# Performance work log

Measured on AMD Instinct MI355X. Metric: run time of the kernel, lower is better.

## Reference

```python
import jax, jax.numpy as jnp
import numpy as np

NUM_ATOMS = 65536
NUM_BONDS = 131072          # directed bonds; row NUM_BONDS is the zero sentinel h(-1)
MAX_NBR = 4
ATOM_FDIM = 133
CONCAT_FDIM = 147           # atom_fdim + bond_fdim
D_HIDDEN = 300
DEPTH = 3
GF_DIM = 2048
N_MOLS = 4096               # uniform molecules: 16 atoms each


def setup_inputs() -> dict:
    key = jax.random.key(0)
    ks = jax.random.split(key, 9)
    atom_features = jax.random.normal(ks[0], (NUM_ATOMS, ATOM_FDIM), dtype=jnp.float32)
    f_ini_atoms_bonds = jax.random.normal(ks[1], (NUM_BONDS + 1, CONCAT_FDIM), dtype=jnp.float32)
    f_ini_atoms_bonds = f_ini_atoms_bonds.at[-1].set(0.0)  # h(-1) sentinel row
    # indices in [-1, NUM_BONDS-1]; -1 means 'no incoming bond' -> sentinel
    mapping = jax.random.randint(ks[2], (NUM_BONDS + 1, MAX_NBR), -1, NUM_BONDS)
    mapping = mapping.at[-1].set(-1)
    atom_to_incoming_bonds = jax.random.randint(ks[3], (NUM_ATOMS, MAX_NBR), -1, NUM_BONDS)
    global_features = jax.random.normal(ks[4], (N_MOLS, GF_DIM), dtype=jnp.float32)
    W_i = jax.random.normal(ks[5], (D_HIDDEN, CONCAT_FDIM), dtype=jnp.float32) / np.sqrt(CONCAT_FDIM)
    W_h = jax.random.normal(ks[6], (D_HIDDEN, D_HIDDEN), dtype=jnp.float32) / np.sqrt(D_HIDDEN)
    W_o = jax.random.normal(ks[7], (D_HIDDEN, ATOM_FDIM + D_HIDDEN), dtype=jnp.float32) / np.sqrt(ATOM_FDIM + D_HIDDEN)
    b_o = jax.random.normal(ks[8], (D_HIDDEN,), dtype=jnp.float32) * 0.01
    return {
        'atom_features': atom_features,
        'f_ini_atoms_bonds': f_ini_atoms_bonds,
        'atom_to_incoming_bonds': atom_to_incoming_bonds,
        'mapping': mapping,
        'global_features': global_features,
        'W_i': W_i, 'W_h': W_h, 'W_o': W_o, 'b_o': b_o,
    }


def reference(atom_features, f_ini_atoms_bonds, atom_to_incoming_bonds, mapping,
              global_features, W_i, W_h, W_o, b_o):
    nb1 = f_ini_atoms_bonds.shape[0]          # num_bonds + 1 (last row = zero sentinel)
    sentinel = nb1 - 1
    # -1 padding indexes the zero sentinel row (torch negative-index trick)
    map_idx = jnp.where(mapping < 0, sentinel, mapping)
    a2b_idx = jnp.where(atom_to_incoming_bonds < 0, sentinel, atom_to_incoming_bonds)

    inp = f_ini_atoms_bonds @ W_i.T           # [nb1, d_hidden]
    h_message = jax.nn.relu(inp)
    for _ in range(1, DEPTH):                 # depth-1 message passing steps
        message = h_message[map_idx].sum(axis=1)          # gather-sum over incoming bonds
        h_message = jax.nn.relu(inp + message @ W_h.T)    # (dropout p=0 omitted)

    # atom readout: sum incoming bond hidden states per atom
    messages = h_message[a2b_idx].sum(axis=1)             # [num_atoms, d_hidden]
    atoms_hidden = jax.nn.relu(
        jnp.concatenate([atom_features, messages], axis=1) @ W_o.T + b_o)

    # mean readout per molecule (uniform molecule size)
    n_mols = global_features.shape[0]
    d = atoms_hidden.shape[-1]
    mol_vecs = atoms_hidden.reshape(n_mols, -1, d).mean(axis=1)
    return jnp.concatenate([mol_vecs, global_features], axis=1)
```

## Files before the change

kernel.cpp:

```cpp
#include <hip/hip_runtime.h>

typedef short bf16x8 __attribute__((ext_vector_type(8)));
typedef float f32x4 __attribute__((ext_vector_type(4)));

constexpr int NB1    = 131073;
constexpr int SENT   = 131072;
constexpr int NATOMS = 65536;
constexpr int AFD    = 133;
constexpr int CFD    = 147;
constexpr int DH     = 300;
constexpr int GFD    = 2048;
constexpr int NMOLS  = 4096;
constexpr int OUTD   = DH + GFD;
constexpr int HS     = 320;
constexpr int KP1    = 160;
constexpr int KP2    = 320;
constexpr int KPC    = 480;

__device__ __forceinline__ unsigned short f2b(float f) {
    unsigned u = __float_as_uint(f);
    u += 0x7fffu + ((u >> 16) & 1u);
    return (unsigned short)(u >> 16);
}
__device__ __forceinline__ float blo(unsigned x) { return __uint_as_float(x << 16); }
__device__ __forceinline__ float bhi(unsigned x) { return __uint_as_float(x & 0xffff0000u); }
__device__ __forceinline__ unsigned pk2(float hi, float lo) {
    return ((unsigned)f2b(hi) << 16) | (unsigned)f2b(lo);
}
__device__ __forceinline__ unsigned pairsum4(unsigned a, unsigned b, unsigned c, unsigned d) {
    float lo = blo(a) + blo(b) + blo(c) + blo(d);
    float hi = bhi(a) + bhi(b) + bhi(c) + bhi(d);
    return pk2(hi, lo);
}
__device__ __forceinline__ unsigned relu_pk(unsigned u) {
    unsigned lo = (u & 0x8000u) ? 0u : (u & 0xFFFFu);
    unsigned hi = (u & 0x80000000u) ? 0u : (u & 0xFFFF0000u);
    return lo | hi;
}
__device__ __forceinline__ uint4 relu4(uint4 v) {
    v.x = relu_pk(v.x); v.y = relu_pk(v.y); v.z = relu_pk(v.z); v.w = relu_pk(v.w);
    return v;
}
__device__ __forceinline__ bf16x8 asbf(uint4 u) {
    union { uint4 u; bf16x8 b; } c; c.u = u; return c.b;
}

__device__ __forceinline__ void mfma_step(const short* __restrict__ A, const uint4 (&B)[5],
                                          int ml, int kl, f32x4 (&acc)[4][5]) {
    bf16x8 af[4];
#pragma unroll
    for (int mt = 0; mt < 4; ++mt)
        af[mt] = *(const bf16x8*)&A[(kl * 64 + mt * 16 + ml) * 8];
#pragma unroll
    for (int mt = 0; mt < 4; ++mt)
#pragma unroll
        for (int nt = 0; nt < 5; ++nt)
            acc[mt][nt] = __builtin_amdgcn_mfma_f32_16x16x32_bf16(af[mt], asbf(B[nt]), acc[mt][nt], 0, 0, 0);
}


__global__ __launch_bounds__(256, 3) void gemm1(
    const float* __restrict__ fini,
    const unsigned short* __restrict__ WiP,
    unsigned short* __restrict__ inp)
{
    __shared__ __align__(16) short As[2][4 * 64 * 8];
    const int tid = threadIdx.x, w = tid >> 6, lane = tid & 63;
    const int ml = lane & 15, kl = lane >> 4;
    const int sr = tid & 63, seg = tid >> 6;
    const int m0 = blockIdx.x * 64;
    const bool mok = (m0 + sr) < NB1;
    const float* fp = fini + (size_t)(mok ? m0 + sr : SENT) * CFD;
    const unsigned short* bp = WiP + (size_t)(w * 80 + ml) * KP1 + kl * 8;

    f32x4 acc[4][5];
#pragma unroll
    for (int mt = 0; mt < 4; ++mt)
#pragma unroll
        for (int nt = 0; nt < 5; ++nt) acc[mt][nt] = (f32x4){0.f, 0.f, 0.f, 0.f};

    {
        union { short s[8]; uint4 u; } st;
#pragma unroll
        for (int j = 0; j < 8; ++j) {
            int k = seg * 8 + j;
            st.s[j] = (short)f2b((mok && k < CFD) ? fp[k] : 0.f);
        }
        *(uint4*)&As[0][(seg * 64 + sr) * 8] = st.u;
    }
    uint4 Bcur[5];
#pragma unroll
    for (int nt = 0; nt < 5; ++nt) Bcur[nt] = *(const uint4*)(bp + nt * 16 * KP1);
    __syncthreads();

    for (int c = 0; c < 5; ++c) {
        const int cn = c + 1;
        float vn[8]; uint4 Bn[5];
        if (cn < 5) {
#pragma unroll
            for (int j = 0; j < 8; ++j) {
                int k = cn * 32 + seg * 8 + j;
                vn[j] = (mok && k < CFD) ? fp[k] : 0.f;
            }
#pragma unroll
            for (int nt = 0; nt < 5; ++nt) Bn[nt] = *(const uint4*)(bp + cn * 32 + nt * 16 * KP1);
        }
        mfma_step(As[c & 1], Bcur, ml, kl, acc);
        if (cn < 5) {
            union { short s[8]; uint4 u; } st;
#pragma unroll
            for (int j = 0; j < 8; ++j) st.s[j] = (short)f2b(vn[j]);
            *(uint4*)&As[cn & 1][(seg * 64 + sr) * 8] = st.u;
#pragma unroll
            for (int nt = 0; nt < 5; ++nt) Bcur[nt] = Bn[nt];
        }
        __syncthreads();
    }
#pragma unroll
    for (int mt = 0; mt < 4; ++mt)
#pragma unroll
        for (int reg = 0; reg < 4; ++reg) {
            int m = m0 + mt * 16 + kl * 4 + reg;
            if (m < NB1) {
#pragma unroll
                for (int nt = 0; nt < 5; ++nt)
                    inp[(size_t)m * HS + w * 80 + nt * 16 + ml] = f2b(acc[mt][nt][reg]);
            }
        }
}

__global__ __launch_bounds__(256, 3) void ygemm(
    const unsigned short* __restrict__ src,
    const unsigned short* __restrict__ Wh,
    unsigned short* __restrict__ y,
    int relu_stage)
{
    __shared__ __align__(16) short As[2][4 * 64 * 8];
    const int tid = threadIdx.x, w = tid >> 6, lane = tid & 63;
    const int ml = lane & 15, kl = lane >> 4;
    const int sr = tid & 63, seg = tid >> 6;
    const int m0 = blockIdx.x * 64;
    const int srow = (m0 + sr) < NB1 ? (m0 + sr) : SENT;
    const unsigned short* ap = src + (size_t)srow * HS + seg * 8;
    const unsigned short* bp = Wh + (size_t)(w * 80 + ml) * KP2 + kl * 8;

    f32x4 acc[4][5];
#pragma unroll
    for (int mt = 0; mt < 4; ++mt)
#pragma unroll
        for (int nt = 0; nt < 5; ++nt) acc[mt][nt] = (f32x4){0.f, 0.f, 0.f, 0.f};

    {
        uint4 av = *(const uint4*)ap;
        if (relu_stage) av = relu4(av);
        *(uint4*)&As[0][(seg * 64 + sr) * 8] = av;
    }
    uint4 Bcur[5];
#pragma unroll
    for (int nt = 0; nt < 5; ++nt) Bcur[nt] = *(const uint4*)(bp + nt * 16 * KP2);
    __syncthreads();

    for (int c = 0; c < 10; ++c) {
        uint4 an; uint4 Bn[5];
        if (c < 9) {
            an = *(const uint4*)(ap + (c + 1) * 32);
#pragma unroll
            for (int nt = 0; nt < 5; ++nt)
                Bn[nt] = *(const uint4*)(bp + (c + 1) * 32 + nt * 16 * KP2);
        }
        mfma_step(As[c & 1], Bcur, ml, kl, acc);
        if (c < 9) {
            if (relu_stage) an = relu4(an);
            *(uint4*)&As[(c + 1) & 1][(seg * 64 + sr) * 8] = an;
#pragma unroll
            for (int nt = 0; nt < 5; ++nt) Bcur[nt] = Bn[nt];
        }
        __syncthreads();
    }
#pragma unroll
    for (int mt = 0; mt < 4; ++mt)
#pragma unroll
        for (int reg = 0; reg < 4; ++reg) {
            int m = m0 + mt * 16 + kl * 4 + reg;
            if (m < NB1) {
#pragma unroll
                for (int nt = 0; nt < 5; ++nt)
                    y[(size_t)m * HS + w * 80 + nt * 16 + ml] = f2b(acc[mt][nt][reg]);
            }
        }
}

__global__ __launch_bounds__(256) void gather_bond(
    const unsigned short* __restrict__ y, const unsigned short* __restrict__ inp,
    const int* __restrict__ mapping, unsigned short* __restrict__ hout)
{
    int t = blockIdx.x * 256 + threadIdx.x;
    int row = t >> 3, g = t & 7;
    if (row >= NB1) return;
    int4 mp = *(const int4*)(mapping + (size_t)row * 4);
    const unsigned short* r0 = y + (size_t)(mp.x < 0 ? SENT : mp.x) * HS;
    const unsigned short* r1 = y + (size_t)(mp.y < 0 ? SENT : mp.y) * HS;
    const unsigned short* r2 = y + (size_t)(mp.z < 0 ? SENT : mp.z) * HS;
    const unsigned short* r3 = y + (size_t)(mp.w < 0 ? SENT : mp.w) * HS;
    const unsigned short* ip = inp + (size_t)row * HS;
    unsigned short* op = hout + (size_t)row * HS;
#pragma unroll
    for (int s = 0; s < 5; ++s) {
        int off = (g + s * 8) * 8;
        uint4 a = *(const uint4*)(r0 + off);
        uint4 b = *(const uint4*)(r1 + off);
        uint4 c = *(const uint4*)(r2 + off);
        uint4 d = *(const uint4*)(r3 + off);
        uint4 e = *(const uint4*)(ip + off);
        uint4 o;
        {
            float lo, hi;
            lo = blo(a.x)+blo(b.x)+blo(c.x)+blo(d.x)+blo(e.x); hi = bhi(a.x)+bhi(b.x)+bhi(c.x)+bhi(d.x)+bhi(e.x);
            o.x = pk2(hi > 0.f ? hi : 0.f, lo > 0.f ? lo : 0.f);
            lo = blo(a.y)+blo(b.y)+blo(c.y)+blo(d.y)+blo(e.y); hi = bhi(a.y)+bhi(b.y)+bhi(c.y)+bhi(d.y)+bhi(e.y);
            o.y = pk2(hi > 0.f ? hi : 0.f, lo > 0.f ? lo : 0.f);
            lo = blo(a.z)+blo(b.z)+blo(c.z)+blo(d.z)+blo(e.z); hi = bhi(a.z)+bhi(b.z)+bhi(c.z)+bhi(d.z)+bhi(e.z);
            o.z = pk2(hi > 0.f ? hi : 0.f, lo > 0.f ? lo : 0.f);
            lo = blo(a.w)+blo(b.w)+blo(c.w)+blo(d.w)+blo(e.w); hi = bhi(a.w)+bhi(b.w)+bhi(c.w)+bhi(d.w)+bhi(e.w);
            o.w = pk2(hi > 0.f ? hi : 0.f, lo > 0.f ? lo : 0.f);
        }
        *(uint4*)(op + off) = o;
    }
}

__global__ __launch_bounds__(256) void gather_atom(
    const unsigned short* __restrict__ h, const int* __restrict__ a2b,
    unsigned short* __restrict__ msg)
{
    int t = blockIdx.x * 256 + threadIdx.x;
    int row = t >> 3, g = t & 7;
    int4 mp = *(const int4*)(a2b + (size_t)row * 4);
    const unsigned short* r0 = h + (size_t)(mp.x < 0 ? SENT : mp.x) * HS;
    const unsigned short* r1 = h + (size_t)(mp.y < 0 ? SENT : mp.y) * HS;
    const unsigned short* r2 = h + (size_t)(mp.z < 0 ? SENT : mp.z) * HS;
    const unsigned short* r3 = h + (size_t)(mp.w < 0 ? SENT : mp.w) * HS;
    unsigned short* op = msg + (size_t)row * HS;
#pragma unroll
    for (int s = 0; s < 5; ++s) {
        int off = (g + s * 8) * 8;
        uint4 a = *(const uint4*)(r0 + off);
        uint4 b = *(const uint4*)(r1 + off);
        uint4 c = *(const uint4*)(r2 + off);
        uint4 d = *(const uint4*)(r3 + off);
        uint4 o;
        o.x = pairsum4(a.x, b.x, c.x, d.x);
        o.y = pairsum4(a.y, b.y, c.y, d.y);
        o.z = pairsum4(a.z, b.z, c.z, d.z);
        o.w = pairsum4(a.w, b.w, c.w, d.w);
        *(uint4*)(op + off) = o;
    }
}

__global__ __launch_bounds__(256, 3) void atom_gemm(
    const float* __restrict__ atomf,
    const unsigned short* __restrict__ msg,
    const unsigned short* __restrict__ WoC,
    const float* __restrict__ bo,
    float* __restrict__ out)
{
    __shared__ __align__(16) short As[2][4 * 64 * 8];
    const int tid = threadIdx.x, w = tid >> 6, lane = tid & 63;
    const int ml = lane & 15, kl = lane >> 4;
    const int sr = tid & 63, seg = tid >> 6;
    const int m0 = blockIdx.x * 64;
    const float* fp = atomf + (size_t)(m0 + sr) * AFD;
    const unsigned short* mp = msg + (size_t)(m0 + sr) * HS + seg * 8;
    const unsigned short* bp = WoC + (size_t)(w * 80 + ml) * KPC + kl * 8;

    f32x4 acc[4][5];
#pragma unroll
    for (int mt = 0; mt < 4; ++mt)
#pragma unroll
        for (int nt = 0; nt < 5; ++nt) acc[mt][nt] = (f32x4){0.f, 0.f, 0.f, 0.f};

    {
        union { short s[8]; uint4 u; } st;
#pragma unroll
        for (int j = 0; j < 8; ++j) {
            int k = seg * 8 + j;
            st.s[j] = (short)f2b(k < AFD ? fp[k] : 0.f);
        }
        *(uint4*)&As[0][(seg * 64 + sr) * 8] = st.u;
    }
    uint4 Bcur[5];
#pragma unroll
    for (int nt = 0; nt < 5; ++nt) Bcur[nt] = *(const uint4*)(bp + nt * 16 * KPC);
    __syncthreads();

    for (int c = 0; c < 15; ++c) {
        const int cn = c + 1;
        float vn[8]; uint4 an; uint4 Bn[5];
        if (cn < 15) {
            if (cn < 5) {
#pragma unroll
                for (int j = 0; j < 8; ++j) {
                    int k = cn * 32 + seg * 8 + j;
                    vn[j] = (k < AFD) ? fp[k] : 0.f;
                }
            } else {
                an = *(const uint4*)(mp + (cn - 5) * 32);
            }
#pragma unroll
            for (int nt = 0; nt < 5; ++nt) Bn[nt] = *(const uint4*)(bp + cn * 32 + nt * 16 * KPC);
        }
        mfma_step(As[c & 1], Bcur, ml, kl, acc);
        if (cn < 15) {
            if (cn < 5) {
                union { short s[8]; uint4 u; } st;
#pragma unroll
                for (int j = 0; j < 8; ++j) st.s[j] = (short)f2b(vn[j]);
                *(uint4*)&As[cn & 1][(seg * 64 + sr) * 8] = st.u;
            } else {
                *(uint4*)&As[cn & 1][(seg * 64 + sr) * 8] = an;
            }
#pragma unroll
            for (int nt = 0; nt < 5; ++nt) Bcur[nt] = Bn[nt];
        }
        __syncthreads();
    }

#pragma unroll
    for (int mt = 0; mt < 4; ++mt) {
        int mol = blockIdx.x * 4 + mt;
#pragma unroll
        for (int nt = 0; nt < 5; ++nt) {
            int n = w * 80 + nt * 16 + ml;
            float bias = (n < DH) ? bo[n] : 0.f;
            float s = 0.f;
#pragma unroll
            for (int reg = 0; reg < 4; ++reg) {
                float v = acc[mt][nt][reg] + bias;
                s += (v > 0.f ? v : 0.f);
            }
            s += __shfl_down(s, 32, 64);
            s += __shfl_down(s, 16, 64);
            if (kl == 0 && n < DH) out[(size_t)mol * OUTD + n] = s * (1.f / 16.f);
        }
    }
}


__global__ __launch_bounds__(256, 3) void bond_gemm_fb(
    const float* __restrict__ fini, const unsigned short* __restrict__ finiB,
    const unsigned short* __restrict__ hsrc, const int* __restrict__ mapping,
    const unsigned short* __restrict__ WiP, const unsigned short* __restrict__ WhP,
    unsigned short* __restrict__ hdst, int do_msg, int useB)
{
    const int tid = threadIdx.x, wv = tid >> 6, lane = tid & 63;
    const int ml = lane & 15, kh = lane >> 4;
    const int m0 = blockIdx.x * 64 + wv * 16;
    const int mrow = m0 + ml;
    const int mrowc = mrow < NB1 ? mrow : SENT;

    f32x4 acc[20];
#pragma unroll
    for (int nt = 0; nt < 20; ++nt) acc[nt] = (f32x4){0.f, 0.f, 0.f, 0.f};

    if (useB) {
        const unsigned short* fb = finiB + (size_t)mrowc * KP1 + kh * 8;
#pragma unroll
        for (int c = 0; c < 5; ++c) {
            bf16x8 af = *(const bf16x8*)(fb + c * 32);
            const unsigned short* bp = WiP + ml * KP1 + c * 32 + kh * 8;
#pragma unroll
            for (int nt = 0; nt < 20; ++nt)
                acc[nt] = __builtin_amdgcn_mfma_f32_16x16x32_bf16(af, *(const bf16x8*)(bp + nt * 16 * KP1), acc[nt], 0, 0, 0);
        }
    } else {
        const float* fp = fini + (size_t)mrowc * CFD;
#pragma unroll
        for (int c = 0; c < 5; ++c) {
            union { short s[8]; bf16x8 x; } u;
#pragma unroll
            for (int j = 0; j < 8; ++j) {
                int k = c * 32 + kh * 8 + j;
                u.s[j] = (short)f2b(k < CFD ? fp[k] : 0.f);
            }
            const unsigned short* bp = WiP + ml * KP1 + c * 32 + kh * 8;
#pragma unroll
            for (int nt = 0; nt < 20; ++nt)
                acc[nt] = __builtin_amdgcn_mfma_f32_16x16x32_bf16(u.x, *(const bf16x8*)(bp + nt * 16 * KP1), acc[nt], 0, 0, 0);
        }
    }
    if (do_msg) {
        int4 mp = *(const int4*)(mapping + (size_t)mrowc * 4);
        const unsigned short* g0 = hsrc + (size_t)(mp.x < 0 ? SENT : mp.x) * HS + kh * 8;
        const unsigned short* g1 = hsrc + (size_t)(mp.y < 0 ? SENT : mp.y) * HS + kh * 8;
        const unsigned short* g2 = hsrc + (size_t)(mp.z < 0 ? SENT : mp.z) * HS + kh * 8;
        const unsigned short* g3 = hsrc + (size_t)(mp.w < 0 ? SENT : mp.w) * HS + kh * 8;
#pragma unroll
        for (int c = 0; c < 10; ++c) {
            uint4 a = *(const uint4*)(g0 + c * 32);
            uint4 b = *(const uint4*)(g1 + c * 32);
            uint4 cc = *(const uint4*)(g2 + c * 32);
            uint4 d = *(const uint4*)(g3 + c * 32);
            uint4 o;
            o.x = pairsum4(a.x, b.x, cc.x, d.x);
            o.y = pairsum4(a.y, b.y, cc.y, d.y);
            o.z = pairsum4(a.z, b.z, cc.z, d.z);
            o.w = pairsum4(a.w, b.w, cc.w, d.w);
            const unsigned short* bp = WhP + ml * KP2 + c * 32 + kh * 8;
#pragma unroll
            for (int nt = 0; nt < 20; ++nt)
                acc[nt] = __builtin_amdgcn_mfma_f32_16x16x32_bf16(asbf(o), *(const bf16x8*)(bp + nt * 16 * KP2), acc[nt], 0, 0, 0);
        }
    }
#pragma unroll
    for (int nt = 0; nt < 20; ++nt) {
        int n = nt * 16 + ml;
#pragma unroll
        for (int reg = 0; reg < 4; ++reg) {
            int m = m0 + kh * 4 + reg;
            if (m < NB1) {
                float v = acc[nt][reg];
                hdst[(size_t)m * HS + n] = f2b(v > 0.f ? v : 0.f);
            }
        }
    }
}

__global__ __launch_bounds__(256, 3) void atom_gemm_fb(
    const float* __restrict__ atomf, const unsigned short* __restrict__ hsrc,
    const int* __restrict__ a2b, const unsigned short* __restrict__ WoA,
    const unsigned short* __restrict__ WoB, const float* __restrict__ bo,
    float* __restrict__ out)
{
    const int tid = threadIdx.x, wv = tid >> 6, lane = tid & 63;
    const int ml = lane & 15, kh = lane >> 4;
    const int m0 = blockIdx.x * 64 + wv * 16;
    const int arow = m0 + ml;

    f32x4 acc[20];
#pragma unroll
    for (int nt = 0; nt < 20; ++nt) acc[nt] = (f32x4){0.f, 0.f, 0.f, 0.f};
    {
        const float* fp = atomf + (size_t)arow * AFD;
#pragma unroll
        for (int c = 0; c < 5; ++c) {
            union { short s[8]; bf16x8 x; } u;
#pragma unroll
            for (int j = 0; j < 8; ++j) {
                int k = c * 32 + kh * 8 + j;
                u.s[j] = (short)f2b(k < AFD ? fp[k] : 0.f);
            }
            const unsigned short* bp = WoA + ml * KP1 + c * 32 + kh * 8;
#pragma unroll
            for (int nt = 0; nt < 20; ++nt)
                acc[nt] = __builtin_amdgcn_mfma_f32_16x16x32_bf16(u.x, *(const bf16x8*)(bp + nt * 16 * KP1), acc[nt], 0, 0, 0);
        }
    }
    {
        int4 mp = *(const int4*)(a2b + (size_t)arow * 4);
        const unsigned short* g0 = hsrc + (size_t)(mp.x < 0 ? SENT : mp.x) * HS + kh * 8;
        const unsigned short* g1 = hsrc + (size_t)(mp.y < 0 ? SENT : mp.y) * HS + kh * 8;
        const unsigned short* g2 = hsrc + (size_t)(mp.z < 0 ? SENT : mp.z) * HS + kh * 8;
        const unsigned short* g3 = hsrc + (size_t)(mp.w < 0 ? SENT : mp.w) * HS + kh * 8;
#pragma unroll
        for (int c = 0; c < 10; ++c) {
            uint4 a = *(const uint4*)(g0 + c * 32);
            uint4 b = *(const uint4*)(g1 + c * 32);
            uint4 cc = *(const uint4*)(g2 + c * 32);
            uint4 d = *(const uint4*)(g3 + c * 32);
            uint4 o;
            o.x = pairsum4(a.x, b.x, cc.x, d.x);
            o.y = pairsum4(a.y, b.y, cc.y, d.y);
            o.z = pairsum4(a.z, b.z, cc.z, d.z);
            o.w = pairsum4(a.w, b.w, cc.w, d.w);
            const unsigned short* bp = WoB + ml * KP2 + c * 32 + kh * 8;
#pragma unroll
            for (int nt = 0; nt < 20; ++nt)
                acc[nt] = __builtin_amdgcn_mfma_f32_16x16x32_bf16(asbf(o), *(const bf16x8*)(bp + nt * 16 * KP2), acc[nt], 0, 0, 0);
        }
    }
    const int mol = blockIdx.x * 4 + wv;
#pragma unroll
    for (int nt = 0; nt < 20; ++nt) {
        int n = nt * 16 + ml;
        float bias = (n < DH) ? bo[n] : 0.f;
        float s = 0.f;
#pragma unroll
        for (int reg = 0; reg < 4; ++reg) {
            float v = acc[nt][reg] + bias;
            s += (v > 0.f ? v : 0.f);
        }
        s += __shfl_down(s, 32, 64);
        s += __shfl_down(s, 16, 64);
        if (kh == 0 && n < DH) out[(size_t)mol * OUTD + n] = s * (1.f / 16.f);
    }
}

__global__ void prep_fini(const float* __restrict__ fini, unsigned short* __restrict__ finiB) {
    int t = blockIdx.x * blockDim.x + threadIdx.x;
    if (t >= NB1 * 20) return;
    int row = t / 20, g = t % 20;
    const float* src = fini + (size_t)row * CFD;
    union { unsigned short s[8]; uint4 u; } o;
#pragma unroll
    for (int j = 0; j < 8; ++j) {
        int k = g * 8 + j;
        o.s[j] = (k < CFD) ? f2b(src[k]) : (unsigned short)0;
    }
    *(uint4*)(finiB + (size_t)row * KP1 + g * 8) = o.u;
}


__global__ void prep_w(const float* __restrict__ Wi, const float* __restrict__ Wh,
                       const float* __restrict__ Wo, unsigned short* __restrict__ wb, int mode) {
    int t = blockIdx.x * blockDim.x + threadIdx.x;
    if (t >= 307200) return;
    float v = 0.f;
    if (t < 51200) {
        int n = t / 160, k = t % 160;
        if (n < DH && k < CFD) v = Wi[n * CFD + k];
    } else if (t < 153600) {
        int q = t - 51200; int n = q / 320, k = q % 320;
        if (n < DH && k < DH) v = Wh[n * DH + k];
    } else if (mode) {
        int q = t - 153600; int n = q / 480, k = q % 480;
        if (n < DH) {
            if (k < AFD) v = Wo[n * 433 + k];
            else if (k >= 160 && k < 460) v = Wo[n * 433 + AFD + (k - 160)];
        }
    } else if (t < 204800) {
        int q = t - 153600; int n = q / 160, k = q % 160;
        if (n < DH && k < AFD) v = Wo[n * 433 + k];
    } else {
        int q = t - 204800; int n = q / 320, k = q % 320;
        if (n < DH && k < DH) v = Wo[n * 433 + AFD + k];
    }
    wb[t] = f2b(v);
}

__global__ void copy_gf(const float4* __restrict__ gf, float* __restrict__ out) {
    int t = blockIdx.x * blockDim.x + threadIdx.x;
    if (t >= NMOLS * (GFD / 4)) return;
    int mol = t >> 9;
    int g4 = t & 511;
    float4 v = gf[t];
    *(float4*)(out + (size_t)mol * OUTD + DH + g4 * 4) = v;
}

extern "C" void kernel_launch(void* const* d_in, const int* in_sizes, int n_in,
                              void* d_out, int out_size, void* d_ws, size_t ws_size,
                              hipStream_t stream) {
    const float* atomf   = (const float*)d_in[0];
    const float* fini    = (const float*)d_in[1];
    const int*   a2b     = (const int*)d_in[2];
    const int*   mapping = (const int*)d_in[3];
    const float* gf      = (const float*)d_in[4];
    const float* W_i     = (const float*)d_in[5];
    const float* W_h     = (const float*)d_in[6];
    const float* W_o     = (const float*)d_in[7];
    const float* b_o     = (const float*)d_in[8];
    float* out = (float*)d_out;

    char* ws = (char*)d_ws;
    size_t SA = (((size_t)NB1 * HS * 2) + 255) & ~(size_t)255;
    size_t SW = 307200 * 2;
    dim3 blk(256);

    if (ws_size >= 3 * SA + SW) {
        unsigned short* inp  = (unsigned short*)ws;
        unsigned short* bufA = (unsigned short*)(ws + SA);
        unsigned short* bufB = (unsigned short*)(ws + 2 * SA);
        unsigned short* wb   = (unsigned short*)(ws + 3 * SA);
        unsigned short* WiP = wb;
        unsigned short* WhP = wb + 51200;
        unsigned short* WoC = wb + 153600;
        unsigned short* msg = inp;

        prep_w<<<1200, blk, 0, stream>>>(W_i, W_h, W_o, wb, 1);
        gemm1<<<2049, blk, 0, stream>>>(fini, WiP, inp);
        ygemm<<<2049, blk, 0, stream>>>(inp, WhP, bufB, 1);
        gather_bond<<<4097, blk, 0, stream>>>(bufB, inp, mapping, bufA);
        ygemm<<<2049, blk, 0, stream>>>(bufA, WhP, bufB, 0);
        gather_bond<<<4097, blk, 0, stream>>>(bufB, inp, mapping, bufA);
        gather_atom<<<2048, blk, 0, stream>>>(bufA, a2b, msg);
        atom_gemm<<<1024, blk, 0, stream>>>(atomf, msg, WoC, b_o, out);
    } else {
        size_t SF = (size_t)NB1 * KP1 * 2;
        unsigned short* h_a = (unsigned short*)ws;
        unsigned short* h_b = (unsigned short*)(ws + SA);
        unsigned short* wb  = (unsigned short*)(ws + 2 * SA);
        unsigned short* finiB = (unsigned short*)(ws + 2 * SA + SW);
        unsigned short* WiP = wb;
        unsigned short* WhP = wb + 51200;
        unsigned short* WoA = wb + 153600;
        unsigned short* WoB = wb + 204800;
        int useB = (ws_size >= 2 * SA + SW + SF) ? 1 : 0;

        prep_w<<<1200, blk, 0, stream>>>(W_i, W_h, W_o, wb, 0);
        if (useB) prep_fini<<<(NB1 * 20 + 255) / 256, blk, 0, stream>>>(fini, finiB);
        bond_gemm_fb<<<2049, blk, 0, stream>>>(fini, finiB, h_a, mapping, WiP, WhP, h_a, 0, useB);
        bond_gemm_fb<<<2049, blk, 0, stream>>>(fini, finiB, h_a, mapping, WiP, WhP, h_b, 1, useB);
        bond_gemm_fb<<<2049, blk, 0, stream>>>(fini, finiB, h_b, mapping, WiP, WhP, h_a, 1, useB);
        atom_gemm_fb<<<1024, blk, 0, stream>>>(atomf, h_a, a2b, WoA, WoB, b_o, out);
    }
    copy_gf<<<NMOLS * (GFD / 4) / 256, blk, 0, stream>>>((const float4*)gf, out);
}
```

Baseline: 612.5 us.

## Fuse gathers and GEMMs into stage kernels with full-K shared-memory tiles

Merges the input projection with the first W_h GEMM, the first bond gather with the second W_h GEMM, and the atom gather with the output GEMM. Each fused kernel stages a full-K tile (padded stride) in LDS so intermediate message buffers no longer round-trip through global memory. This cuts the launch count and global traffic for two intermediate tensors. In exchange the larger LDS footprint lowers occupancy to 2 blocks per CU and drops the double-buffered prefetch. The fallback path also loses its bf16 pre-converted fini option.

```diff
diff --git a/kernel.cpp b/kernel.cpp
--- a/kernel.cpp
+++ b/kernel.cpp
@@ -16,6 +16,8 @@
 constexpr int KP1    = 160;
 constexpr int KP2    = 320;
 constexpr int KPC    = 480;
+constexpr int LSTR   = 328;
+constexpr int LSTRC  = 488;
 
 __device__ __forceinline__ unsigned short f2b(float f) {
     unsigned u = __float_as_uint(f);
@@ -32,46 +34,22 @@
     float hi = bhi(a) + bhi(b) + bhi(c) + bhi(d);
     return pk2(hi, lo);
 }
-__device__ __forceinline__ unsigned relu_pk(unsigned u) {
-    unsigned lo = (u & 0x8000u) ? 0u : (u & 0xFFFFu);
-    unsigned hi = (u & 0x80000000u) ? 0u : (u & 0xFFFF0000u);
-    return lo | hi;
-}
-__device__ __forceinline__ uint4 relu4(uint4 v) {
-    v.x = relu_pk(v.x); v.y = relu_pk(v.y); v.z = relu_pk(v.z); v.w = relu_pk(v.w);
-    return v;
-}
 __device__ __forceinline__ bf16x8 asbf(uint4 u) {
     union { uint4 u; bf16x8 b; } c; c.u = u; return c.b;
 }
 
-__device__ __forceinline__ void mfma_step(const short* __restrict__ A, const uint4 (&B)[5],
-                                          int ml, int kl, f32x4 (&acc)[4][5]) {
-    bf16x8 af[4];
-#pragma unroll
-    for (int mt = 0; mt < 4; ++mt)
-        af[mt] = *(const bf16x8*)&A[(kl * 64 + mt * 16 + ml) * 8];
-#pragma unroll
-    for (int mt = 0; mt < 4; ++mt)
-#pragma unroll
-        for (int nt = 0; nt < 5; ++nt)
-            acc[mt][nt] = __builtin_amdgcn_mfma_f32_16x16x32_bf16(af[mt], asbf(B[nt]), acc[mt][nt], 0, 0, 0);
-}
-
-
-__global__ __launch_bounds__(256, 3) void gemm1(
+
+__global__ __launch_bounds__(256, 2) void fused_in(
     const float* __restrict__ fini,
     const unsigned short* __restrict__ WiP,
-    unsigned short* __restrict__ inp)
+    const unsigned short* __restrict__ WhP,
+    unsigned short* __restrict__ inp,
+    unsigned short* __restrict__ y1)
 {
-    __shared__ __align__(16) short As[2][4 * 64 * 8];
+    __shared__ __align__(16) short As[64 * LSTR];
     const int tid = threadIdx.x, w = tid >> 6, lane = tid & 63;
     const int ml = lane & 15, kl = lane >> 4;
-    const int sr = tid & 63, seg = tid >> 6;
     const int m0 = blockIdx.x * 64;
-    const bool mok = (m0 + sr) < NB1;
-    const float* fp = fini + (size_t)(mok ? m0 + sr : SENT) * CFD;
-    const unsigned short* bp = WiP + (size_t)(w * 80 + ml) * KP1 + kl * 8;
 
     f32x4 acc[4][5];
 #pragma unroll
@@ -79,42 +57,76 @@
 #pragma unroll
         for (int nt = 0; nt < 5; ++nt) acc[mt][nt] = (f32x4){0.f, 0.f, 0.f, 0.f};
 
-    {
-        union { short s[8]; uint4 u; } st;
-#pragma unroll
-        for (int j = 0; j < 8; ++j) {
-            int k = seg * 8 + j;
-            st.s[j] = (short)f2b((mok && k < CFD) ? fp[k] : 0.f);
-        }
-        *(uint4*)&As[0][(seg * 64 + sr) * 8] = st.u;
-    }
-    uint4 Bcur[5];
-#pragma unroll
-    for (int nt = 0; nt < 5; ++nt) Bcur[nt] = *(const uint4*)(bp + nt * 16 * KP1);
+    const float* fr[4];
+#pragma unroll
+    for (int mt = 0; mt < 4; ++mt) {
+        int r = m0 + mt * 16 + ml;
+        fr[mt] = fini + (size_t)(r < NB1 ? r : SENT) * CFD + kl * 8;
+    }
+    const unsigned short* bpi = WiP + (size_t)(w * 80 + ml) * KP1 + kl * 8;
+#pragma unroll
+    for (int c = 0; c < 5; ++c) {
+        uint4 B[5];
+#pragma unroll
+        for (int nt = 0; nt < 5; ++nt) B[nt] = *(const uint4*)(bpi + c * 32 + nt * 16 * KP1);
+        bf16x8 af[4];
+#pragma unroll
+        for (int mt = 0; mt < 4; ++mt) {
+            union { short s[8]; bf16x8 x; } u;
+            if (c < 4) {
+#pragma unroll
+                for (int j = 0; j < 8; ++j) u.s[j] = (short)f2b(fr[mt][c * 32 + j]);
+            } else {
+#pragma unroll
+                for (int j = 0; j < 8; ++j) {
+                    int k = 128 + kl * 8 + j;
+                    u.s[j] = (short)f2b(k < CFD ? fr[mt][c * 32 + j] : 0.f);
+                }
+            }
+            af[mt] = u.x;
+        }
+#pragma unroll
+        for (int mt = 0; mt < 4; ++mt)
+#pragma unroll
+            for (int nt = 0; nt < 5; ++nt)
+                acc[mt][nt] = __builtin_amdgcn_mfma_f32_16x16x32_bf16(af[mt], asbf(B[nt]), acc[mt][nt], 0, 0, 0);
+    }
+
+#pragma unroll
+    for (int mt = 0; mt < 4; ++mt)
+#pragma unroll
+        for (int reg = 0; reg < 4; ++reg) {
+            int lr = mt * 16 + kl * 4 + reg;
+            int m = m0 + lr;
+#pragma unroll
+            for (int nt = 0; nt < 5; ++nt) {
+                int col = w * 80 + nt * 16 + ml;
+                float v = acc[mt][nt][reg];
+                if (m < NB1) inp[(size_t)m * HS + col] = f2b(v);
+                As[lr * LSTR + col] = (short)f2b(v > 0.f ? v : 0.f);
+            }
+        }
     __syncthreads();
 
-    for (int c = 0; c < 5; ++c) {
-        const int cn = c + 1;
-        float vn[8]; uint4 Bn[5];
-        if (cn < 5) {
-#pragma unroll
-            for (int j = 0; j < 8; ++j) {
-                int k = cn * 32 + seg * 8 + j;
-                vn[j] = (mok && k < CFD) ? fp[k] : 0.f;
-            }
-#pragma unroll
-            for (int nt = 0; nt < 5; ++nt) Bn[nt] = *(const uint4*)(bp + cn * 32 + nt * 16 * KP1);
-        }
-        mfma_step(As[c & 1], Bcur, ml, kl, acc);
-        if (cn < 5) {
-            union { short s[8]; uint4 u; } st;
-#pragma unroll
-            for (int j = 0; j < 8; ++j) st.s[j] = (short)f2b(vn[j]);
-            *(uint4*)&As[cn & 1][(seg * 64 + sr) * 8] = st.u;
-#pragma unroll
-            for (int nt = 0; nt < 5; ++nt) Bcur[nt] = Bn[nt];
-        }
-        __syncthreads();
+#pragma unroll
+    for (int mt = 0; mt < 4; ++mt)
+#pragma unroll
+        for (int nt = 0; nt < 5; ++nt) acc[mt][nt] = (f32x4){0.f, 0.f, 0.f, 0.f};
+    const unsigned short* bph = WhP + (size_t)(w * 80 + ml) * KP2 + kl * 8;
+#pragma unroll
+    for (int c = 0; c < 10; ++c) {
+        uint4 B[5];
+#pragma unroll
+        for (int nt = 0; nt < 5; ++nt) B[nt] = *(const uint4*)(bph + c * 32 + nt * 16 * KP2);
+        bf16x8 af[4];
+#pragma unroll
+        for (int mt = 0; mt < 4; ++mt)
+            af[mt] = *(const bf16x8*)&As[(mt * 16 + ml) * LSTR + c * 32 + kl * 8];
+#pragma unroll
+        for (int mt = 0; mt < 4; ++mt)
+#pragma unroll
+            for (int nt = 0; nt < 5; ++nt)
+                acc[mt][nt] = __builtin_amdgcn_mfma_f32_16x16x32_bf16(af[mt], asbf(B[nt]), acc[mt][nt], 0, 0, 0);
     }
 #pragma unroll
     for (int mt = 0; mt < 4; ++mt)
@@ -124,58 +136,76 @@
             if (m < NB1) {
 #pragma unroll
                 for (int nt = 0; nt < 5; ++nt)
-                    inp[(size_t)m * HS + w * 80 + nt * 16 + ml] = f2b(acc[mt][nt][reg]);
-            }
-        }
-}
-
-__global__ __launch_bounds__(256, 3) void ygemm(
-    const unsigned short* __restrict__ src,
-    const unsigned short* __restrict__ Wh,
-    unsigned short* __restrict__ y,
-    int relu_stage)
+                    y1[(size_t)m * HS + w * 80 + nt * 16 + ml] = f2b(acc[mt][nt][reg]);
+            }
+        }
+}
+
+__global__ __launch_bounds__(256, 2) void fused_mid(
+    const unsigned short* __restrict__ ysrc,
+    const unsigned short* __restrict__ inp,
+    const int* __restrict__ mapping,
+    const unsigned short* __restrict__ WhP,
+    unsigned short* __restrict__ ydst)
 {
-    __shared__ __align__(16) short As[2][4 * 64 * 8];
+    __shared__ __align__(16) short As[64 * LSTR];
     const int tid = threadIdx.x, w = tid >> 6, lane = tid & 63;
     const int ml = lane & 15, kl = lane >> 4;
-    const int sr = tid & 63, seg = tid >> 6;
     const int m0 = blockIdx.x * 64;
-    const int srow = (m0 + sr) < NB1 ? (m0 + sr) : SENT;
-    const unsigned short* ap = src + (size_t)srow * HS + seg * 8;
-    const unsigned short* bp = Wh + (size_t)(w * 80 + ml) * KP2 + kl * 8;
+
+    {
+        const int sr = tid & 63, sg = tid >> 6;
+        int srow = m0 + sr;
+        int crow = srow < NB1 ? srow : SENT;
+        int4 mp = *(const int4*)(mapping + (size_t)crow * 4);
+        const unsigned short* r0 = ysrc + (size_t)(mp.x < 0 ? SENT : mp.x) * HS;
+        const unsigned short* r1 = ysrc + (size_t)(mp.y < 0 ? SENT : mp.y) * HS;
+        const unsigned short* r2 = ysrc + (size_t)(mp.z < 0 ? SENT : mp.z) * HS;
+        const unsigned short* r3 = ysrc + (size_t)(mp.w < 0 ? SENT : mp.w) * HS;
+        const unsigned short* ip = inp + (size_t)crow * HS;
+#pragma unroll
+        for (int s = 0; s < 10; ++s) {
+            int off = (s * 4 + sg) * 8;
+            uint4 a = *(const uint4*)(r0 + off);
+            uint4 b = *(const uint4*)(r1 + off);
+            uint4 c = *(const uint4*)(r2 + off);
+            uint4 d = *(const uint4*)(r3 + off);
+            uint4 e = *(const uint4*)(ip + off);
+            uint4 o;
+            float lo, hi;
+            lo = blo(a.x)+blo(b.x)+blo(c.x)+blo(d.x)+blo(e.x); hi = bhi(a.x)+bhi(b.x)+bhi(c.x)+bhi(d.x)+bhi(e.x);
+            o.x = pk2(hi > 0.f ? hi : 0.f, lo > 0.f ? lo : 0.f);
+            lo = blo(a.y)+blo(b.y)+blo(c.y)+blo(d.y)+blo(e.y); hi = bhi(a.y)+bhi(b.y)+bhi(c.y)+bhi(d.y)+bhi(e.y);
+            o.y = pk2(hi > 0.f ? hi : 0.f, lo > 0.f ? lo : 0.f);
+            lo = blo(a.z)+blo(b.z)+blo(c.z)+blo(d.z)+blo(e.z); hi = bhi(a.z)+bhi(b.z)+bhi(c.z)+bhi(d.z)+bhi(e.z);
+            o.z = pk2(hi > 0.f ? hi : 0.f, lo > 0.f ? lo : 0.f);
+            lo = blo(a.w)+blo(b.w)+blo(c.w)+blo(d.w)+blo(e.w); hi = bhi(a.w)+bhi(b.w)+bhi(c.w)+bhi(d.w)+bhi(e.w);
+            o.w = pk2(hi > 0.f ? hi : 0.f, lo > 0.f ? lo : 0.f);
+            *(uint4*)&As[sr * LSTR + off] = o;
+        }
+    }
+    __syncthreads();
 
     f32x4 acc[4][5];
 #pragma unroll
     for (int mt = 0; mt < 4; ++mt)
 #pragma unroll
         for (int nt = 0; nt < 5; ++nt) acc[mt][nt] = (f32x4){0.f, 0.f, 0.f, 0.f};
-
-    {
-        uint4 av = *(const uint4*)ap;
-        if (relu_stage) av = relu4(av);
-        *(uint4*)&As[0][(seg * 64 + sr) * 8] = av;
-    }
-    uint4 Bcur[5];
-#pragma unroll
-    for (int nt = 0; nt < 5; ++nt) Bcur[nt] = *(const uint4*)(bp + nt * 16 * KP2);
-    __syncthreads();
-
+    const unsigned short* bph = WhP + (size_t)(w * 80 + ml) * KP2 + kl * 8;
+#pragma unroll
     for (int c = 0; c < 10; ++c) {
-        uint4 an; uint4 Bn[5];
-        if (c < 9) {
-            an = *(const uint4*)(ap + (c + 1) * 32);
+        uint4 B[5];
+#pragma unroll
+        for (int nt = 0; nt < 5; ++nt) B[nt] = *(const uint4*)(bph + c * 32 + nt * 16 * KP2);
+        bf16x8 af[4];
+#pragma unroll
+        for (int mt = 0; mt < 4; ++mt)
+            af[mt] = *(const bf16x8*)&As[(mt * 16 + ml) * LSTR + c * 32 + kl * 8];
+#pragma unroll
+        for (int mt = 0; mt < 4; ++mt)
 #pragma unroll
             for (int nt = 0; nt < 5; ++nt)
-                Bn[nt] = *(const uint4*)(bp + (c + 1) * 32 + nt * 16 * KP2);
-        }
-        mfma_step(As[c & 1], Bcur, ml, kl, acc);
-        if (c < 9) {
-            if (relu_stage) an = relu4(an);
-            *(uint4*)&As[(c + 1) & 1][(seg * 64 + sr) * 8] = an;
-#pragma unroll
-            for (int nt = 0; nt < 5; ++nt) Bcur[nt] = Bn[nt];
-        }
-        __syncthreads();
+                acc[mt][nt] = __builtin_amdgcn_mfma_f32_16x16x32_bf16(af[mt], asbf(B[nt]), acc[mt][nt], 0, 0, 0);
     }
 #pragma unroll
     for (int mt = 0; mt < 4; ++mt)
@@ -185,7 +215,7 @@
             if (m < NB1) {
 #pragma unroll
                 for (int nt = 0; nt < 5; ++nt)
-                    y[(size_t)m * HS + w * 80 + nt * 16 + ml] = f2b(acc[mt][nt][reg]);
+                    ydst[(size_t)m * HS + w * 80 + nt * 16 + ml] = f2b(acc[mt][nt][reg]);
             }
         }
 }
@@ -213,115 +243,89 @@
         uint4 d = *(const uint4*)(r3 + off);
         uint4 e = *(const uint4*)(ip + off);
         uint4 o;
-        {
-            float lo, hi;
-            lo = blo(a.x)+blo(b.x)+blo(c.x)+blo(d.x)+blo(e.x); hi = bhi(a.x)+bhi(b.x)+bhi(c.x)+bhi(d.x)+bhi(e.x);
-            o.x = pk2(hi > 0.f ? hi : 0.f, lo > 0.f ? lo : 0.f);
-            lo = blo(a.y)+blo(b.y)+blo(c.y)+blo(d.y)+blo(e.y); hi = bhi(a.y)+bhi(b.y)+bhi(c.y)+bhi(d.y)+bhi(e.y);
-            o.y = pk2(hi > 0.f ? hi : 0.f, lo > 0.f ? lo : 0.f);
-            lo = blo(a.z)+blo(b.z)+blo(c.z)+blo(d.z)+blo(e.z); hi = bhi(a.z)+bhi(b.z)+bhi(c.z)+bhi(d.z)+bhi(e.z);
-            o.z = pk2(hi > 0.f ? hi : 0.f, lo > 0.f ? lo : 0.f);
-            lo = blo(a.w)+blo(b.w)+blo(c.w)+blo(d.w)+blo(e.w); hi = bhi(a.w)+bhi(b.w)+bhi(c.w)+bhi(d.w)+bhi(e.w);
-            o.w = pk2(hi > 0.f ? hi : 0.f, lo > 0.f ? lo : 0.f);
-        }
+        float lo, hi;
+        lo = blo(a.x)+blo(b.x)+blo(c.x)+blo(d.x)+blo(e.x); hi = bhi(a.x)+bhi(b.x)+bhi(c.x)+bhi(d.x)+bhi(e.x);
+        o.x = pk2(hi > 0.f ? hi : 0.f, lo > 0.f ? lo : 0.f);
+        lo = blo(a.y)+blo(b.y)+blo(c.y)+blo(d.y)+blo(e.y); hi = bhi(a.y)+bhi(b.y)+bhi(c.y)+bhi(d.y)+bhi(e.y);
+        o.y = pk2(hi > 0.f ? hi : 0.f, lo > 0.f ? lo : 0.f);
+        lo = blo(a.z)+blo(b.z)+blo(c.z)+blo(d.z)+blo(e.z); hi = bhi(a.z)+bhi(b.z)+bhi(c.z)+bhi(d.z)+bhi(e.z);
+        o.z = pk2(hi > 0.f ? hi : 0.f, lo > 0.f ? lo : 0.f);
+        lo = blo(a.w)+blo(b.w)+blo(c.w)+blo(d.w)+blo(e.w); hi = bhi(a.w)+bhi(b.w)+bhi(c.w)+bhi(d.w)+bhi(e.w);
+        o.w = pk2(hi > 0.f ? hi : 0.f, lo > 0.f ? lo : 0.f);
         *(uint4*)(op + off) = o;
     }
 }
 
-__global__ __launch_bounds__(256) void gather_atom(
-    const unsigned short* __restrict__ h, const int* __restrict__ a2b,
-    unsigned short* __restrict__ msg)
-{
-    int t = blockIdx.x * 256 + threadIdx.x;
-    int row = t >> 3, g = t & 7;
-    int4 mp = *(const int4*)(a2b + (size_t)row * 4);
-    const unsigned short* r0 = h + (size_t)(mp.x < 0 ? SENT : mp.x) * HS;
-    const unsigned short* r1 = h + (size_t)(mp.y < 0 ? SENT : mp.y) * HS;
-    const unsigned short* r2 = h + (size_t)(mp.z < 0 ? SENT : mp.z) * HS;
-    const unsigned short* r3 = h + (size_t)(mp.w < 0 ? SENT : mp.w) * HS;
-    unsigned short* op = msg + (size_t)row * HS;
-#pragma unroll
-    for (int s = 0; s < 5; ++s) {
-        int off = (g + s * 8) * 8;
-        uint4 a = *(const uint4*)(r0 + off);
-        uint4 b = *(const uint4*)(r1 + off);
-        uint4 c = *(const uint4*)(r2 + off);
-        uint4 d = *(const uint4*)(r3 + off);
-        uint4 o;
-        o.x = pairsum4(a.x, b.x, c.x, d.x);
-        o.y = pairsum4(a.y, b.y, c.y, d.y);
-        o.z = pairsum4(a.z, b.z, c.z, d.z);
-        o.w = pairsum4(a.w, b.w, c.w, d.w);
-        *(uint4*)(op + off) = o;
-    }
-}
-
-__global__ __launch_bounds__(256, 3) void atom_gemm(
+__global__ __launch_bounds__(256, 2) void fused_atom(
     const float* __restrict__ atomf,
-    const unsigned short* __restrict__ msg,
+    const unsigned short* __restrict__ h,
+    const int* __restrict__ a2b,
     const unsigned short* __restrict__ WoC,
     const float* __restrict__ bo,
     float* __restrict__ out)
 {
-    __shared__ __align__(16) short As[2][4 * 64 * 8];
+    __shared__ __align__(16) short As[64 * LSTRC];
     const int tid = threadIdx.x, w = tid >> 6, lane = tid & 63;
     const int ml = lane & 15, kl = lane >> 4;
-    const int sr = tid & 63, seg = tid >> 6;
     const int m0 = blockIdx.x * 64;
-    const float* fp = atomf + (size_t)(m0 + sr) * AFD;
-    const unsigned short* mp = msg + (size_t)(m0 + sr) * HS + seg * 8;
+
+    {
+        const int sr = tid & 63, sg = tid >> 6;
+        int row = m0 + sr;
+        int4 mp = *(const int4*)(a2b + (size_t)row * 4);
+        const unsigned short* r0 = h + (size_t)(mp.x < 0 ? SENT : mp.x) * HS;
+        const unsigned short* r1 = h + (size_t)(mp.y < 0 ? SENT : mp.y) * HS;
+        const unsigned short* r2 = h + (size_t)(mp.z < 0 ? SENT : mp.z) * HS;
+        const unsigned short* r3 = h + (size_t)(mp.w < 0 ? SENT : mp.w) * HS;
+        const float* fp = atomf + (size_t)row * AFD;
+#pragma unroll
+        for (int s = 0; s < 15; ++s) {
+            int k0 = (s * 4 + sg) * 8;
+            if (k0 < KP1) {
+                union { short s8[8]; uint4 u; } u;
+#pragma unroll
+                for (int j = 0; j < 8; ++j) {
+                    int k = k0 + j;
+                    u.s8[j] = (short)f2b(k < AFD ? fp[k] : 0.f);
+                }
+                *(uint4*)&As[sr * LSTRC + k0] = u.u;
+            } else {
+                int off = k0 - KP1;
+                uint4 a = *(const uint4*)(r0 + off);
+                uint4 b = *(const uint4*)(r1 + off);
+                uint4 c = *(const uint4*)(r2 + off);
+                uint4 d = *(const uint4*)(r3 + off);
+                uint4 o;
+                o.x = pairsum4(a.x, b.x, c.x, d.x);
+                o.y = pairsum4(a.y, b.y, c.y, d.y);
+                o.z = pairsum4(a.z, b.z, c.z, d.z);
+                o.w = pairsum4(a.w, b.w, c.w, d.w);
+                *(uint4*)&As[sr * LSTRC + k0] = o;
+            }
+        }
+    }
+    __syncthreads();
+
+    f32x4 acc[4][5];
+#pragma unroll
+    for (int mt = 0; mt < 4; ++mt)
+#pragma unroll
+        for (int nt = 0; nt < 5; ++nt) acc[mt][nt] = (f32x4){0.f, 0.f, 0.f, 0.f};
     const unsigned short* bp = WoC + (size_t)(w * 80 + ml) * KPC + kl * 8;
-
-    f32x4 acc[4][5];
-#pragma unroll
-    for (int mt = 0; mt < 4; ++mt)
-#pragma unroll
-        for (int nt = 0; nt < 5; ++nt) acc[mt][nt] = (f32x4){0.f, 0.f, 0.f, 0.f};
-
-    {
-        union { short s[8]; uint4 u; } st;
-#pragma unroll
-        for (int j = 0; j < 8; ++j) {
-            int k = seg * 8 + j;
-            st.s[j] = (short)f2b(k < AFD ? fp[k] : 0.f);
-        }
-        *(uint4*)&As[0][(seg * 64 + sr) * 8] = st.u;
-    }
-    uint4 Bcur[5];
-#pragma unroll
-    for (int nt = 0; nt < 5; ++nt) Bcur[nt] = *(const uint4*)(bp + nt * 16 * KPC);
-    __syncthreads();
-
+#pragma unroll
     for (int c = 0; c < 15; ++c) {
-        const int cn = c + 1;
-        float vn[8]; uint4 an; uint4 Bn[5];
-        if (cn < 15) {
-            if (cn < 5) {
-#pragma unroll
-                for (int j = 0; j < 8; ++j) {
-                    int k = cn * 32 + seg * 8 + j;
-                    vn[j] = (k < AFD) ? fp[k] : 0.f;
-                }
-            } else {
-                an = *(const uint4*)(mp + (cn - 5) * 32);
-            }
-#pragma unroll
-            for (int nt = 0; nt < 5; ++nt) Bn[nt] = *(const uint4*)(bp + cn * 32 + nt * 16 * KPC);
-        }
-        mfma_step(As[c & 1], Bcur, ml, kl, acc);
-        if (cn < 15) {
-            if (cn < 5) {
-                union { short s[8]; uint4 u; } st;
-#pragma unroll
-                for (int j = 0; j < 8; ++j) st.s[j] = (short)f2b(vn[j]);
-                *(uint4*)&As[cn & 1][(seg * 64 + sr) * 8] = st.u;
-            } else {
-                *(uint4*)&As[cn & 1][(seg * 64 + sr) * 8] = an;
-            }
-#pragma unroll
-            for (int nt = 0; nt < 5; ++nt) Bcur[nt] = Bn[nt];
-        }
-        __syncthreads();
+        uint4 B[5];
+#pragma unroll
+        for (int nt = 0; nt < 5; ++nt) B[nt] = *(const uint4*)(bp + c * 32 + nt * 16 * KPC);
+        bf16x8 af[4];
+#pragma unroll
+        for (int mt = 0; mt < 4; ++mt)
+            af[mt] = *(const bf16x8*)&As[(mt * 16 + ml) * LSTRC + c * 32 + kl * 8];
+#pragma unroll
+        for (int mt = 0; mt < 4; ++mt)
+#pragma unroll
+            for (int nt = 0; nt < 5; ++nt)
+                acc[mt][nt] = __builtin_amdgcn_mfma_f32_16x16x32_bf16(af[mt], asbf(B[nt]), acc[mt][nt], 0, 0, 0);
     }
 
 #pragma unroll
@@ -346,10 +350,10 @@
 
 
 __global__ __launch_bounds__(256, 3) void bond_gemm_fb(
-    const float* __restrict__ fini, const unsigned short* __restrict__ finiB,
-    const unsigned short* __restrict__ hsrc, const int* __restrict__ mapping,
-    const unsigned short* __restrict__ WiP, const unsigned short* __restrict__ WhP,
-    unsigned short* __restrict__ hdst, int do_msg, int useB)
+    const float* __restrict__ fini, const unsigned short* __restrict__ hsrc,
+    const int* __restrict__ mapping, const unsigned short* __restrict__ WiP,
+    const unsigned short* __restrict__ WhP, unsigned short* __restrict__ hdst,
+    int do_msg)
 {
     const int tid = threadIdx.x, wv = tid >> 6, lane = tid & 63;
     const int ml = lane & 15, kh = lane >> 4;
@@ -360,18 +364,7 @@
     f32x4 acc[20];
 #pragma unroll
     for (int nt = 0; nt < 20; ++nt) acc[nt] = (f32x4){0.f, 0.f, 0.f, 0.f};
-
-    if (useB) {
-        const unsigned short* fb = finiB + (size_t)mrowc * KP1 + kh * 8;
-#pragma unroll
-        for (int c = 0; c < 5; ++c) {
-            bf16x8 af = *(const bf16x8*)(fb + c * 32);
-            const unsigned short* bp = WiP + ml * KP1 + c * 32 + kh * 8;
-#pragma unroll
-            for (int nt = 0; nt < 20; ++nt)
-                acc[nt] = __builtin_amdgcn_mfma_f32_16x16x32_bf16(af, *(const bf16x8*)(bp + nt * 16 * KP1), acc[nt], 0, 0, 0);
-        }
-    } else {
+    {
         const float* fp = fini + (size_t)mrowc * CFD;
 #pragma unroll
         for (int c = 0; c < 5; ++c) {
@@ -492,20 +485,6 @@
         s += __shfl_down(s, 16, 64);
         if (kh == 0 && n < DH) out[(size_t)mol * OUTD + n] = s * (1.f / 16.f);
     }
-}
-
-__global__ void prep_fini(const float* __restrict__ fini, unsigned short* __restrict__ finiB) {
-    int t = blockIdx.x * blockDim.x + threadIdx.x;
-    if (t >= NB1 * 20) return;
-    int row = t / 20, g = t % 20;
-    const float* src = fini + (size_t)row * CFD;
-    union { unsigned short s[8]; uint4 u; } o;
-#pragma unroll
-    for (int j = 0; j < 8; ++j) {
-        int k = g * 8 + j;
-        o.s[j] = (k < CFD) ? f2b(src[k]) : (unsigned short)0;
-    }
-    *(uint4*)(finiB + (size_t)row * KP1 + g * 8) = o.u;
 }
 
 
@@ -565,40 +544,33 @@
     dim3 blk(256);
 
     if (ws_size >= 3 * SA + SW) {
-        unsigned short* inp  = (unsigned short*)ws;
-        unsigned short* bufA = (unsigned short*)(ws + SA);
-        unsigned short* bufB = (unsigned short*)(ws + 2 * SA);
-        unsigned short* wb   = (unsigned short*)(ws + 3 * SA);
+        unsigned short* inp = (unsigned short*)ws;
+        unsigned short* y1  = (unsigned short*)(ws + SA);
+        unsigned short* y2  = (unsigned short*)(ws + 2 * SA);
+        unsigned short* wb  = (unsigned short*)(ws + 3 * SA);
         unsigned short* WiP = wb;
         unsigned short* WhP = wb + 51200;
         unsigned short* WoC = wb + 153600;
-        unsigned short* msg = inp;
+        unsigned short* h2  = y1;
 
         prep_w<<<1200, blk, 0, stream>>>(W_i, W_h, W_o, wb, 1);
-        gemm1<<<2049, blk, 0, stream>>>(fini, WiP, inp);
-        ygemm<<<2049, blk, 0, stream>>>(inp, WhP, bufB, 1);
-        gather_bond<<<4097, blk, 0, stream>>>(bufB, inp, mapping, bufA);
-        ygemm<<<2049, blk, 0, stream>>>(bufA, WhP, bufB, 0);
-        gather_bond<<<4097, blk, 0, stream>>>(bufB, inp, mapping, bufA);
-        gather_atom<<<2048, blk, 0, stream>>>(bufA, a2b, msg);
-        atom_gemm<<<1024, blk, 0, stream>>>(atomf, msg, WoC, b_o, out);
+        fused_in<<<2049, blk, 0, stream>>>(fini, WiP, WhP, inp, y1);
+        fused_mid<<<2049, blk, 0, stream>>>(y1, inp, mapping, WhP, y2);
+        gather_bond<<<4097, blk, 0, stream>>>(y2, inp, mapping, h2);
+        fused_atom<<<1024, blk, 0, stream>>>(atomf, h2, a2b, WoC, b_o, out);
     } else {
-        size_t SF = (size_t)NB1 * KP1 * 2;
         unsigned short* h_a = (unsigned short*)ws;
         unsigned short* h_b = (unsigned short*)(ws + SA);
         unsigned short* wb  = (unsigned short*)(ws + 2 * SA);
-        unsigned short* finiB = (unsigned short*)(ws + 2 * SA + SW);
         unsigned short* WiP = wb;
         unsigned short* WhP = wb + 51200;
         unsigned short* WoA = wb + 153600;
         unsigned short* WoB = wb + 204800;
-        int useB = (ws_size >= 2 * SA + SW + SF) ? 1 : 0;
 
         prep_w<<<1200, blk, 0, stream>>>(W_i, W_h, W_o, wb, 0);
-        if (useB) prep_fini<<<(NB1 * 20 + 255) / 256, blk, 0, stream>>>(fini, finiB);
-        bond_gemm_fb<<<2049, blk, 0, stream>>>(fini, finiB, h_a, mapping, WiP, WhP, h_a, 0, useB);
-        bond_gemm_fb<<<2049, blk, 0, stream>>>(fini, finiB, h_a, mapping, WiP, WhP, h_b, 1, useB);
-        bond_gemm_fb<<<2049, blk, 0, stream>>>(fini, finiB, h_b, mapping, WiP, WhP, h_a, 1, useB);
+        bond_gemm_fb<<<2049, blk, 0, stream>>>(fini, h_a, mapping, WiP, WhP, h_a, 0);
+        bond_gemm_fb<<<2049, blk, 0, stream>>>(fini, h_a, mapping, WiP, WhP, h_b, 1);
+        bond_gemm_fb<<<2049, blk, 0, stream>>>(fini, h_b, mapping, WiP, WhP, h_a, 1);
         atom_gemm_fb<<<1024, blk, 0, stream>>>(atomf, h_a, a2b, WoA, WoB, b_o, out);
     }
     copy_gf<<<NMOLS * (GFD / 4) / 256, blk, 0, stream>>>((const float4*)gf, out);
```

Measured after the change: 584.3 us. 1.05x faster.
